# Kernel tuning notes

Hardware: AMD Instinct MI355X
Metric: run time of the kernel (lower is better)

## Reference

```python
import jax, jax.numpy as jnp
import numpy as np

T, B, D, V, E = 512, 128, 512, 33, 128  # time, batch, hidden/enc dim, vocab, embed dim


def setup_inputs() -> dict:
    key = jax.random.key(0)
    ks = jax.random.split(key, 9)
    s = 0.05  # weight init scale, keeps activations sane
    return {
        "enc_h": jax.random.normal(ks[0], (T, B, D), dtype=jnp.float32),
        "W_emb": jax.random.normal(ks[1], (V, E), dtype=jnp.float32) * s,
        "b_emb": jax.random.normal(ks[2], (E,), dtype=jnp.float32) * s,
        "W_ih": jax.random.normal(ks[3], (E, 4 * D), dtype=jnp.float32) * s,
        "W_hh": jax.random.normal(ks[4], (D, 4 * D), dtype=jnp.float32) * s,
        "b_ih": jax.random.normal(ks[5], (4 * D,), dtype=jnp.float32) * s,
        "b_hh": jax.random.normal(ks[6], (4 * D,), dtype=jnp.float32) * s,
        "W_out": jax.random.normal(ks[7], (2 * D, V), dtype=jnp.float32) * s,
        "b_out": jax.random.normal(ks[8], (V,), dtype=jnp.float32) * s,
    }


def reference(enc_h, W_emb, b_emb, W_ih, W_hh, b_ih, b_hh, W_out, b_out):
    # self.y is a zeros buffer that is never updated, so the embed output is
    # constant across timesteps: embed(zeros) = b_emb broadcast to [B, E].
    y_emb = jnp.zeros((B, V), enc_h.dtype) @ W_emb + b_emb  # [B, E]

    def lstm_cell(x, h, c):
        g = x @ W_ih + b_ih + h @ W_hh + b_hh  # [B, 4D]
        i, f, gg, o = jnp.split(g, 4, axis=-1)  # torch LSTMCell gate order
        i, f, o = jax.nn.sigmoid(i), jax.nn.sigmoid(f), jax.nn.sigmoid(o)
        c_new = f * c + i * jnp.tanh(gg)
        h_new = o * jnp.tanh(c_new)
        return h_new, c_new

    def step(carry, hidden):  # hidden: [B, D]
        h, c, c_t = carry
        h, c = lstm_cell(y_emb, h, c)
        # Attention (faithful to the original, including raw-score denominator):
        score = hidden.T @ h                                   # [D, D]
        a_t = jnp.exp(score) / jnp.sum(score, axis=0)          # [D, D]
        # the python loop `for a in a_t: c_t += a * h_e` == sum rows, broadcast
        w = jnp.sum(a_t, axis=0)                               # [D]
        c_t = c_t + w[None, :] * hidden                        # [B, D] (stateful buffer)
        comb = jnp.concatenate([h, c_t], axis=1)               # [B, 2D]
        y_hat = jax.nn.log_softmax(comb @ W_out + b_out, axis=1)
        return (h, c, c_t), y_hat

    init = (jnp.zeros((B, D), enc_h.dtype),
            jnp.zeros((B, D), enc_h.dtype),
            jnp.zeros((B, D), enc_h.dtype))
    _, preds = jax.lax.scan(step, init, enc_h)  # [T, B, V]
    return preds
```

## Files before the change

### kernel.cpp

```cpp
#include <hip/hip_runtime.h>
#include <math.h>

constexpr int T_ = 512, B_ = 128, D_ = 512, V_ = 33, E_ = 128;
constexpr int G4 = 4 * D_;
constexpr int BD = B_ * D_;
constexpr int BV = B_ * V_;
constexpr int TWO_D = 2 * D_;
constexpr int WIMG_HALF = 1048576;

typedef __attribute__((ext_vector_type(8))) short short8;
typedef __attribute__((ext_vector_type(4))) float floatx4;

__device__ inline short f2bf(float f) {
    unsigned u = __float_as_uint(f);
    unsigned r = (u + 0x7fff + ((u >> 16) & 1)) >> 16;
    return (short)r;
}
__device__ inline float bf2f(short s) {
    return __uint_as_float(((unsigned)(unsigned short)s) << 16);
}

__global__ void prep_kernel(const float* __restrict__ b_emb, const float* __restrict__ W_ih,
                            const float* __restrict__ b_ih, const float* __restrict__ b_hh,
                            const float* __restrict__ W_out,
                            float* __restrict__ g0, float* __restrict__ WoT) {
    int idx = blockIdx.x * 256 + threadIdx.x;
    if (idx < G4) {
        float acc = b_ih[idx] + b_hh[idx];
        for (int e = 0; e < E_; ++e) acc = fmaf(b_emb[e], W_ih[e * G4 + idx], acc);
        g0[idx] = acc;
    } else {
        int k = idx - G4;
        if (k < V_ * TWO_D) {
            int v = k / TWO_D, j = k % TWO_D;
            WoT[v * TWO_D + j] = W_out[j * V_ + v];
        }
    }
}

__global__ void prep2_kernel(const float* __restrict__ Whh, short* __restrict__ Wimg) {
    int idx = blockIdx.x * 256 + threadIdx.x;
    int G = idx & 2047, k = idx >> 11;
    float v = Whh[(size_t)k * G4 + G];
    short hi = f2bf(v);
    short lo = f2bf(v - bf2f(hi));
    int g = G >> 9, cc = G & 511, n = cc >> 4, c = cc & 15;
    int kt = k >> 5, kg = (k >> 3) & 3, j = k & 7;
    int lane = kg * 16 + c;
    size_t dst = ((size_t)((n * 4 + g) * 16 + kt) * 64 + lane) * 8 + j;
    Wimg[dst] = hi;
    Wimg[dst + WIMG_HALF] = lo;
}

__global__ void rowsum_kernel(const float* __restrict__ enc, double* __restrict__ rowsum) {
    int wave = threadIdx.x >> 6, lane = threadIdx.x & 63;
    int row = blockIdx.x * 4 + wave;
    const float* p = enc + (size_t)row * D_;
    double s = 0.0;
    #pragma unroll
    for (int k = 0; k < 8; ++k) s += (double)p[k * 64 + lane];
    for (int off = 32; off; off >>= 1) s += __shfl_down(s, off, 64);
    if (lane == 0) rowsum[row] = s;
}

__global__ void __launch_bounds__(256, 1) lstm_step(const short* __restrict__ Wimg,
                                                    const float* __restrict__ g0,
                                                    float* __restrict__ Hs,
                                                    short* __restrict__ hb,
                                                    int t) {
    __shared__ short Alds[16384];
    __shared__ float xch[3][64][4];
    const int tid = threadIdx.x;
    const int l = tid & 63, g = tid >> 6;
    const int m = blockIdx.x & 7, n = blockIdx.x >> 3;
    const int col = l & 15, kg = l >> 4;
    const float g0v = g0[g * 512 + n * 16 + col];
    const short* __restrict__ bbase = Wimg + ((size_t)((n * 4 + g) * 16) * 64 + l) * 8;

    floatx4 acc = {0.f, 0.f, 0.f, 0.f};
    if (t > 0) {
        {
            const short* ah = hb + (size_t)((t - 1) & 1) * 131072 + m * 8192;
            const short* al = ah + 65536;
            #pragma unroll
            for (int it = 0; it < 4; ++it) {
                int u = it * 256 + tid;
                int s = (u & ~63) | ((u & 63) ^ ((u >> 6) & 7));
                *(short8*)&Alds[s * 8]        = *(const short8*)&ah[u * 8];
                *(short8*)&Alds[8192 + s * 8] = *(const short8*)&al[u * 8];
            }
        }
        __syncthreads();
        #pragma unroll
        for (int kt = 0; kt < 16; ++kt) {
            int sA = ((col << 6) | ((kt * 4 + kg) ^ (col & 7))) * 8;
            short8 ahi = *(const short8*)&Alds[sA];
            short8 alo = *(const short8*)&Alds[8192 + sA];
            short8 bh = *(const short8*)(bbase + kt * 512);
            short8 bl = *(const short8*)(bbase + WIMG_HALF + kt * 512);
            acc = __builtin_amdgcn_mfma_f32_16x16x32_bf16(ahi, bh, acc, 0, 0, 0);
            acc = __builtin_amdgcn_mfma_f32_16x16x32_bf16(ahi, bl, acc, 0, 0, 0);
            acc = __builtin_amdgcn_mfma_f32_16x16x32_bf16(alo, bh, acc, 0, 0, 0);
        }
    }
    if (g > 0) {
        xch[g - 1][l][0] = acc[0] + g0v;
        xch[g - 1][l][1] = acc[1] + g0v;
        xch[g - 1][l][2] = acc[2] + g0v;
        xch[g - 1][l][3] = acc[3] + g0v;
    }
    __syncthreads();
    if (g == 0) {
        float ip[4], fp[4], gp[4], op[4];
        #pragma unroll
        for (int j = 0; j < 4; ++j) {
            ip[j] = acc[j] + g0v;
            fp[j] = xch[0][l][j];
            gp[j] = xch[1][l][j];
            op[j] = xch[2][l][j];
        }
        float* cst = (float*)(hb + 2 * 131072);
        short* hw = hb + (size_t)(t & 1) * 131072;
        #pragma unroll
        for (int j = 0; j < 4; ++j) {
            int row = m * 16 + kg * 4 + j;
            int pos = row * 512 + n * 16 + col;
            float i_ = 1.f / (1.f + expf(-ip[j]));
            float f_ = 1.f / (1.f + expf(-fp[j]));
            float gg = tanhf(gp[j]);
            float o_ = 1.f / (1.f + expf(-op[j]));
            float cprev = (t > 0) ? cst[pos] : 0.f;
            float c_new = f_ * cprev + i_ * gg;
            cst[pos] = c_new;
            float h = o_ * tanhf(c_new);
            Hs[(size_t)t * BD + pos] = h;
            short hi = f2bf(h);
            short lo = f2bf(h - bf2f(hi));
            hw[pos] = hi;
            hw[65536 + pos] = lo;
        }
    }
}

__global__ void score_kernel(const float* __restrict__ enc, const float* __restrict__ Hs,
                             const double* __restrict__ rowsum, float* __restrict__ wout) {
    __shared__ float Hj[B_][68];
    __shared__ float Ei[B_][36];
    __shared__ float numer[64];
    const int tid = threadIdx.x;
    const int t  = blockIdx.x >> 3;
    const int j0 = (blockIdx.x & 7) * 64;
    for (int i = 0; i < 32; ++i) {
        int idx = i * 256 + tid;
        int bb = idx >> 6, jl = idx & 63;
        Hj[bb][jl] = Hs[(size_t)t * BD + bb * D_ + j0 + jl];
    }
    if (tid < 64) numer[tid] = 0.f;
    __syncthreads();
    const int ti = tid & 15;
    const int tj = tid >> 4;
    for (int itile = 0; itile < 16; ++itile) {
        int i0 = itile * 32;
        for (int i = 0; i < 16; ++i) {
            int idx = i * 256 + tid;
            int bb = idx >> 5, il = idx & 31;
            Ei[bb][il] = enc[(size_t)t * BD + bb * D_ + i0 + il];
        }
        __syncthreads();
        float a00=0,a01=0,a02=0,a03=0,a10=0,a11=0,a12=0,a13=0;
        #pragma unroll 4
        for (int bb = 0; bb < B_; ++bb) {
            float2 e2 = *(const float2*)&Ei[bb][ti * 2];
            float4 h4 = *(const float4*)&Hj[bb][tj * 4];
            a00 = fmaf(e2.x, h4.x, a00); a01 = fmaf(e2.x, h4.y, a01);
            a02 = fmaf(e2.x, h4.z, a02); a03 = fmaf(e2.x, h4.w, a03);
            a10 = fmaf(e2.y, h4.x, a10); a11 = fmaf(e2.y, h4.y, a11);
            a12 = fmaf(e2.y, h4.z, a12); a13 = fmaf(e2.y, h4.w, a13);
        }
        float v0 = expf(a00) + expf(a10);
        float v1 = expf(a01) + expf(a11);
        float v2 = expf(a02) + expf(a12);
        float v3 = expf(a03) + expf(a13);
        #pragma unroll
        for (int off = 1; off < 16; off <<= 1) {
            v0 += __shfl_xor(v0, off, 16);
            v1 += __shfl_xor(v1, off, 16);
            v2 += __shfl_xor(v2, off, 16);
            v3 += __shfl_xor(v3, off, 16);
        }
        if (ti == 0) {
            numer[tj * 4 + 0] += v0;
            numer[tj * 4 + 1] += v1;
            numer[tj * 4 + 2] += v2;
            numer[tj * 4 + 3] += v3;
        }
        __syncthreads();
    }
    if (tid < 64) {
        const double* rs = rowsum + t * B_;
        double dd = 0.0;
        for (int bb = 0; bb < B_; ++bb) dd += rs[bb] * (double)Hj[bb][tid];
        wout[t * D_ + j0 + tid] = (float)((double)numer[tid] / dd);
    }
}

__global__ void ufuse_kernel(const float* __restrict__ enc, const float* __restrict__ Hs,
                             const float* __restrict__ wbuf, const float* __restrict__ WoT,
                             float* __restrict__ u, float* __restrict__ hlog) {
    int wave = threadIdx.x >> 6, lane = threadIdx.x & 63;
    int row = blockIdx.x * 4 + wave;
    int t = row >> 7, b = row & 127;
    const float* Erow = enc + (size_t)row * D_;
    const float* Hrow = Hs  + (size_t)row * D_;
    const float* wrow = wbuf + t * D_;
    float ar[8], hr[8];
    #pragma unroll
    for (int k = 0; k < 8; ++k) {
        int j = k * 64 + lane;
        ar[k] = wrow[j] * Erow[j];
        hr[k] = Hrow[j];
    }
    for (int v = 0; v < V_; ++v) {
        const float* wo = WoT + v * TWO_D;
        float su = 0.f, sh = 0.f;
        #pragma unroll
        for (int k = 0; k < 8; ++k) {
            int j = k * 64 + lane;
            su = fmaf(ar[k], wo[D_ + j], su);
            sh = fmaf(hr[k], wo[j], sh);
        }
        for (int off = 32; off; off >>= 1) {
            su += __shfl_down(su, off, 64);
            sh += __shfl_down(sh, off, 64);
        }
        if (lane == 0) {
            u[(size_t)t * BV + b * V_ + v] = su;
            hlog[(size_t)row * V_ + v] = sh;
        }
    }
}

__global__ void cumsum_kernel(float* __restrict__ u) {
    int bv = blockIdx.x * 256 + threadIdx.x;
    if (bv >= BV) return;
    float acc = 0.f;
    for (int t = 0; t < T_; ++t) {
        acc += u[(size_t)t * BV + bv];
        u[(size_t)t * BV + bv] = acc;
    }
}

__global__ void final_kernel(const float* __restrict__ hlog, const float* __restrict__ u,
                             const float* __restrict__ b_out, float* __restrict__ out) {
    int row = blockIdx.x * 256 + threadIdx.x;
    float logit[V_];
    float m = -INFINITY;
    #pragma unroll
    for (int v = 0; v < V_; ++v) {
        float x = hlog[(size_t)row * V_ + v] + u[(size_t)row * V_ + v] + b_out[v];
        logit[v] = x;
        m = fmaxf(m, x);
    }
    float s = 0.f;
    #pragma unroll
    for (int v = 0; v < V_; ++v) s += expf(logit[v] - m);
    float lse = m + logf(s);
    #pragma unroll
    for (int v = 0; v < V_; ++v) out[(size_t)row * V_ + v] = logit[v] - lse;
}

extern "C" void kernel_launch(void* const* d_in, const int* in_sizes, int n_in,
                              void* d_out, int out_size, void* d_ws, size_t ws_size,
                              hipStream_t stream) {
    const float* enc   = (const float*)d_in[0];
    const float* b_emb = (const float*)d_in[2];
    const float* W_ih  = (const float*)d_in[3];
    const float* W_hh  = (const float*)d_in[4];
    const float* b_ih  = (const float*)d_in[5];
    const float* b_hh  = (const float*)d_in[6];
    const float* W_out = (const float*)d_in[7];
    const float* b_out = (const float*)d_in[8];
    float* out = (float*)d_out;

    char* p = (char*)d_ws;
    double* rowsum = (double*)p;              p += sizeof(double) * (size_t)T_ * B_;
    float* Hs      = (float*)p;               p += sizeof(float) * (size_t)T_ * BD;
    float* wbuf    = (float*)p;               p += sizeof(float) * (size_t)T_ * D_;
    float* u       = (float*)p;               p += sizeof(float) * (size_t)T_ * BV;
    float* hlog    = (float*)p;               p += sizeof(float) * (size_t)T_ * BV;
    float* g0      = (float*)p;               p += sizeof(float) * G4;
    float* WoT     = (float*)p;               p += sizeof(float) * V_ * TWO_D;
    short* Wimg    = (short*)p;               p += sizeof(short) * 2 * WIMG_HALF;
    short* hb      = (short*)p;               p += sizeof(short) * (2 * 131072 + 2 * BD);

    prep_kernel<<<(G4 + V_ * TWO_D + 255) / 256, 256, 0, stream>>>(b_emb, W_ih, b_ih, b_hh, W_out, g0, WoT);
    prep2_kernel<<<(G4 * D_) / 256, 256, 0, stream>>>(W_hh, Wimg);
    rowsum_kernel<<<T_ * B_ / 4, 256, 0, stream>>>(enc, rowsum);
    for (int t = 0; t < T_; ++t) {
        lstm_step<<<256, 256, 0, stream>>>(Wimg, g0, Hs, hb, t);
    }
    score_kernel<<<T_ * 8, 256, 0, stream>>>(enc, Hs, rowsum, wbuf);
    ufuse_kernel<<<T_ * B_ / 4, 256, 0, stream>>>(enc, Hs, wbuf, WoT, u, hlog);
    cumsum_kernel<<<(BV + 255) / 256, 256, 0, stream>>>(u);
    final_kernel<<<T_ * B_ / 256, 256, 0, stream>>>(hlog, u, b_out, out);
}
```

Baseline: 5.133 ms.

## Replace per-timestep LSTM launches with persistent cooperative kernel and flag barriers

Turns the 512 per-step lstm_step launches into one cooperative persistent kernel that loops over time. Blocks sharing a batch tile sync through per-step atomic counters in global memory. The cell state is kept in registers, and h's hi/lo bf16 halves are packed into one 32-bit word. Gate math is spread across all four waves instead of only wave 0. This removes launch overhead and global cell-state traffic, at the cost of spin-wait latency and a reliance on all 256 blocks being co-resident.

```diff
diff --git a/kernel.cpp b/kernel.cpp
--- a/kernel.cpp
+++ b/kernel.cpp
@@ -1,4 +1,5 @@
 #include <hip/hip_runtime.h>
+#include <hip/hip_cooperative_groups.h>
 #include <math.h>
 
 constexpr int T_ = 512, B_ = 128, D_ = 512, V_ = 33, E_ = 128;
@@ -63,81 +64,105 @@
     if (lane == 0) rowsum[row] = s;
 }
 
-__global__ void __launch_bounds__(256, 1) lstm_step(const short* __restrict__ Wimg,
-                                                    const float* __restrict__ g0,
-                                                    float* __restrict__ Hs,
-                                                    short* __restrict__ hb,
-                                                    int t) {
+__global__ void __launch_bounds__(256, 1) lstm_persist(const short* __restrict__ Wimg,
+                                                       const float* __restrict__ g0,
+                                                       float* __restrict__ Hs,
+                                                       unsigned* __restrict__ hpack,
+                                                       unsigned* __restrict__ bar) {
     __shared__ short Alds[16384];
-    __shared__ float xch[3][64][4];
+    __shared__ float xch[4][64][4];
     const int tid = threadIdx.x;
     const int l = tid & 63, g = tid >> 6;
     const int m = blockIdx.x & 7, n = blockIdx.x >> 3;
     const int col = l & 15, kg = l >> 4;
     const float g0v = g0[g * 512 + n * 16 + col];
     const short* __restrict__ bbase = Wimg + ((size_t)((n * 4 + g) * 16) * 64 + l) * 8;
-
-    floatx4 acc = {0.f, 0.f, 0.f, 0.f};
-    if (t > 0) {
+    const int erow = m * 16 + kg * 4 + g;
+    const int epos = erow * 512 + n * 16 + col;
+    float creg = 0.f;
+
+    for (int t = 0; t < T_; ++t) {
+        floatx4 acc = {0.f, 0.f, 0.f, 0.f};
+        if (t > 0) {
+            if (l == 0) {
+                const unsigned* flag = bar + (size_t)((t - 1) * 8 + m) * 16;
+                while (__hip_atomic_load(flag, __ATOMIC_RELAXED, __HIP_MEMORY_SCOPE_AGENT) < 32u) {
+                    __builtin_amdgcn_s_sleep(2);
+                }
+            }
+            __syncthreads();
+            {
+                const unsigned* src = hpack + (size_t)((t - 1) & 1) * 65536 + m * 8192;
+                #pragma unroll
+                for (int it = 0; it < 4; ++it) {
+                    int u = it * 256 + tid;
+                    int s = (u & ~63) | ((u & 63) ^ ((u >> 6) & 7));
+                    const unsigned long long* qp = (const unsigned long long*)(src + u * 8);
+                    unsigned long long d0 = __hip_atomic_load(qp + 0, __ATOMIC_RELAXED, __HIP_MEMORY_SCOPE_AGENT);
+                    unsigned long long d1 = __hip_atomic_load(qp + 1, __ATOMIC_RELAXED, __HIP_MEMORY_SCOPE_AGENT);
+                    unsigned long long d2 = __hip_atomic_load(qp + 2, __ATOMIC_RELAXED, __HIP_MEMORY_SCOPE_AGENT);
+                    unsigned long long d3 = __hip_atomic_load(qp + 3, __ATOMIC_RELAXED, __HIP_MEMORY_SCOPE_AGENT);
+                    unsigned p0 = (unsigned)d0, p1 = (unsigned)(d0 >> 32);
+                    unsigned p2 = (unsigned)d1, p3 = (unsigned)(d1 >> 32);
+                    unsigned p4 = (unsigned)d2, p5 = (unsigned)(d2 >> 32);
+                    unsigned p6 = (unsigned)d3, p7 = (unsigned)(d3 >> 32);
+                    uint4 hiq, loq;
+                    hiq.x = (p1 & 0xFFFF0000u) | (p0 >> 16);
+                    hiq.y = (p3 & 0xFFFF0000u) | (p2 >> 16);
+                    hiq.z = (p5 & 0xFFFF0000u) | (p4 >> 16);
+                    hiq.w = (p7 & 0xFFFF0000u) | (p6 >> 16);
+                    loq.x = (p1 << 16) | (p0 & 0xFFFFu);
+                    loq.y = (p3 << 16) | (p2 & 0xFFFFu);
+                    loq.z = (p5 << 16) | (p4 & 0xFFFFu);
+                    loq.w = (p7 << 16) | (p6 & 0xFFFFu);
+                    *(uint4*)&Alds[s * 8]        = hiq;
+                    *(uint4*)&Alds[8192 + s * 8] = loq;
+                }
+            }
+            __syncthreads();
+            #pragma unroll
+            for (int kt = 0; kt < 16; ++kt) {
+                int sA = ((col << 6) | ((kt * 4 + kg) ^ (col & 7))) * 8;
+                short8 ahi = *(const short8*)&Alds[sA];
+                short8 alo = *(const short8*)&Alds[8192 + sA];
+                short8 bh = *(const short8*)(bbase + kt * 512);
+                short8 bl = *(const short8*)(bbase + WIMG_HALF + kt * 512);
+                acc = __builtin_amdgcn_mfma_f32_16x16x32_bf16(ahi, bh, acc, 0, 0, 0);
+                acc = __builtin_amdgcn_mfma_f32_16x16x32_bf16(ahi, bl, acc, 0, 0, 0);
+                acc = __builtin_amdgcn_mfma_f32_16x16x32_bf16(alo, bh, acc, 0, 0, 0);
+            }
+        }
+        xch[g][l][0] = acc[0] + g0v;
+        xch[g][l][1] = acc[1] + g0v;
+        xch[g][l][2] = acc[2] + g0v;
+        xch[g][l][3] = acc[3] + g0v;
+        __syncthreads();
         {
-            const short* ah = hb + (size_t)((t - 1) & 1) * 131072 + m * 8192;
-            const short* al = ah + 65536;
-            #pragma unroll
-            for (int it = 0; it < 4; ++it) {
-                int u = it * 256 + tid;
-                int s = (u & ~63) | ((u & 63) ^ ((u >> 6) & 7));
-                *(short8*)&Alds[s * 8]        = *(const short8*)&ah[u * 8];
-                *(short8*)&Alds[8192 + s * 8] = *(const short8*)&al[u * 8];
-            }
-        }
-        __syncthreads();
-        #pragma unroll
-        for (int kt = 0; kt < 16; ++kt) {
-            int sA = ((col << 6) | ((kt * 4 + kg) ^ (col & 7))) * 8;
-            short8 ahi = *(const short8*)&Alds[sA];
-            short8 alo = *(const short8*)&Alds[8192 + sA];
-            short8 bh = *(const short8*)(bbase + kt * 512);
-            short8 bl = *(const short8*)(bbase + WIMG_HALF + kt * 512);
-            acc = __builtin_amdgcn_mfma_f32_16x16x32_bf16(ahi, bh, acc, 0, 0, 0);
-            acc = __builtin_amdgcn_mfma_f32_16x16x32_bf16(ahi, bl, acc, 0, 0, 0);
-            acc = __builtin_amdgcn_mfma_f32_16x16x32_bf16(alo, bh, acc, 0, 0, 0);
-        }
-    }
-    if (g > 0) {
-        xch[g - 1][l][0] = acc[0] + g0v;
-        xch[g - 1][l][1] = acc[1] + g0v;
-        xch[g - 1][l][2] = acc[2] + g0v;
-        xch[g - 1][l][3] = acc[3] + g0v;
-    }
-    __syncthreads();
-    if (g == 0) {
-        float ip[4], fp[4], gp[4], op[4];
-        #pragma unroll
-        for (int j = 0; j < 4; ++j) {
-            ip[j] = acc[j] + g0v;
-            fp[j] = xch[0][l][j];
-            gp[j] = xch[1][l][j];
-            op[j] = xch[2][l][j];
-        }
-        float* cst = (float*)(hb + 2 * 131072);
-        short* hw = hb + (size_t)(t & 1) * 131072;
-        #pragma unroll
-        for (int j = 0; j < 4; ++j) {
-            int row = m * 16 + kg * 4 + j;
-            int pos = row * 512 + n * 16 + col;
-            float i_ = 1.f / (1.f + expf(-ip[j]));
-            float f_ = 1.f / (1.f + expf(-fp[j]));
-            float gg = tanhf(gp[j]);
-            float o_ = 1.f / (1.f + expf(-op[j]));
-            float cprev = (t > 0) ? cst[pos] : 0.f;
-            float c_new = f_ * cprev + i_ * gg;
-            cst[pos] = c_new;
+            float ip = xch[0][l][g];
+            float fp = xch[1][l][g];
+            float gp = xch[2][l][g];
+            float op = xch[3][l][g];
+            float i_ = 1.f / (1.f + expf(-ip));
+            float f_ = 1.f / (1.f + expf(-fp));
+            float gg = tanhf(gp);
+            float o_ = 1.f / (1.f + expf(-op));
+            float c_new = f_ * creg + i_ * gg;
+            creg = c_new;
             float h = o_ * tanhf(c_new);
-            Hs[(size_t)t * BD + pos] = h;
+            Hs[(size_t)t * BD + epos] = h;
             short hi = f2bf(h);
             short lo = f2bf(h - bf2f(hi));
-            hw[pos] = hi;
-            hw[65536 + pos] = lo;
+            unsigned pk = ((unsigned)(unsigned short)hi << 16) | (unsigned)(unsigned short)lo;
+            __hip_atomic_store(&hpack[(size_t)(t & 1) * 65536 + epos], pk,
+                               __ATOMIC_RELAXED, __HIP_MEMORY_SCOPE_AGENT);
+        }
+        if (t + 1 < T_) {
+            asm volatile("s_waitcnt vmcnt(0)" ::: "memory");
+            __syncthreads();
+            if (tid == 0) {
+                __hip_atomic_fetch_add(bar + (size_t)(t * 8 + m) * 16, 1u,
+                                       __ATOMIC_RELAXED, __HIP_MEMORY_SCOPE_AGENT);
+            }
         }
     }
 }
@@ -291,13 +316,21 @@
     float* g0      = (float*)p;               p += sizeof(float) * G4;
     float* WoT     = (float*)p;               p += sizeof(float) * V_ * TWO_D;
     short* Wimg    = (short*)p;               p += sizeof(short) * 2 * WIMG_HALF;
-    short* hb      = (short*)p;               p += sizeof(short) * (2 * 131072 + 2 * BD);
-
+    unsigned* hpack = (unsigned*)p;           p += sizeof(unsigned) * 2 * BD;
+    unsigned* bar  = (unsigned*)p;            p += sizeof(unsigned) * T_ * 8 * 16;
+
+    hipMemsetAsync(bar, 0, sizeof(unsigned) * T_ * 8 * 16, stream);
     prep_kernel<<<(G4 + V_ * TWO_D + 255) / 256, 256, 0, stream>>>(b_emb, W_ih, b_ih, b_hh, W_out, g0, WoT);
     prep2_kernel<<<(G4 * D_) / 256, 256, 0, stream>>>(W_hh, Wimg);
     rowsum_kernel<<<T_ * B_ / 4, 256, 0, stream>>>(enc, rowsum);
-    for (int t = 0; t < T_; ++t) {
-        lstm_step<<<256, 256, 0, stream>>>(Wimg, g0, Hs, hb, t);
+    {
+        const short* Wimg_p = Wimg;
+        const float* g0_p   = g0;
+        float* Hs_p = Hs;
+        unsigned* hpack_p = hpack;
+        unsigned* bar_p = bar;
+        void* args[] = { (void*)&Wimg_p, (void*)&g0_p, (void*)&Hs_p, (void*)&hpack_p, (void*)&bar_p };
+        hipLaunchCooperativeKernel(lstm_persist, dim3(256), dim3(256), args, 0, stream);
     }
     score_kernel<<<T_ * 8, 256, 0, stream>>>(enc, Hs, rowsum, wbuf);
     ufuse_kernel<<<T_ * B_ / 4, 256, 0, stream>>>(enc, Hs, wbuf, WoT, u, hlog);
```

Result: slower. 6.001 ms (+16.9%).
